# Kernel optimization log

Measured on AMD Instinct MI355X. Metric: run time of the kernel, lower is better.

## Reference

```python
import jax, jax.numpy as jnp
import numpy as np

DIM, HEADS, WIN, SHIFT = 384, 12, 7, 3
H, W = 56, 56
HEAD_DIM = DIM // HEADS
SCALE = HEAD_DIM ** -0.5
N = WIN * WIN


def _relative_index():
    coords = np.stack(np.meshgrid(np.arange(WIN), np.arange(WIN), indexing='ij')).reshape(2, -1)
    rel = (coords[:, :, None] - coords[:, None, :]).transpose(1, 2, 0)
    rel[:, :, 0] += WIN - 1
    rel[:, :, 1] += WIN - 1
    rel[:, :, 0] *= 2 * WIN - 1
    return rel.sum(-1)  # [N, N] int


def _attn_mask():
    img = np.zeros((H, W), dtype=np.float32)
    cnt = 0
    sls = (slice(0, -WIN), slice(-WIN, -SHIFT), slice(-SHIFT, None))
    for hs in sls:
        for ws in sls:
            img[hs, ws] = cnt
            cnt += 1
    m = img.reshape(H // WIN, WIN, W // WIN, WIN).transpose(0, 2, 1, 3).reshape(-1, N)  # [nw, N]
    diff = m[:, None, :] - m[:, :, None]  # [nw, N, N]
    return np.where(diff != 0, -10000.0, 0.0).astype(np.float32)

REL_IDX = jnp.asarray(_relative_index())
MASK = jnp.asarray(_attn_mask())  # [nw, N, N]


def _layernorm(x, w, b):
    mu = x.mean(-1, keepdims=True)
    var = ((x - mu) ** 2).mean(-1, keepdims=True)
    return (x - mu) * jax.lax.rsqrt(var + 1e-5) * w + b


def _window_partition(x):  # [B,H,W,C] -> [B*nw, N, C]
    B, _, _, C = x.shape
    x = x.reshape(B, H // WIN, WIN, W // WIN, WIN, C)
    x = x.transpose(0, 1, 3, 2, 4, 5)
    return x.reshape(-1, N, C)


def _window_reverse(w, B):  # [B*nw, N, C] -> [B,H,W,C]
    C = w.shape[-1]
    x = w.reshape(B, H // WIN, W // WIN, WIN, WIN, C)
    x = x.transpose(0, 1, 3, 2, 4, 5)
    return x.reshape(B, H, W, C)


def setup_inputs() -> dict:
    key = jax.random.key(0)
    ks = jax.random.split(key, 12)
    s = DIM ** -0.5
    return {
        'x': jax.random.normal(ks[0], (32, H * W, DIM), jnp.float32),
        'qkv_w': jax.random.normal(ks[1], (DIM, 3 * DIM), jnp.float32) * s,  # stored [in,out]
        'qkv_b': jnp.zeros((3 * DIM,), jnp.float32),
        'proj_w': jax.random.normal(ks[2], (DIM, DIM), jnp.float32) * s,
        'proj_b': jnp.zeros((DIM,), jnp.float32),
        'rel_bias': jax.random.normal(ks[3], ((2 * WIN - 1) ** 2, HEADS), jnp.float32) * 0.02,
        'norm1_w': jnp.ones((DIM,), jnp.float32),
        'norm1_b': jnp.zeros((DIM,), jnp.float32),
        'norm2_w': jnp.ones((DIM,), jnp.float32),
        'norm2_b': jnp.zeros((DIM,), jnp.float32),
        'mlp_w1': jax.random.normal(ks[4], (DIM, 4 * DIM), jnp.float32) * s,
        'mlp_b1': jnp.zeros((4 * DIM,), jnp.float32),
        'mlp_w2': jax.random.normal(ks[5], (4 * DIM, DIM), jnp.float32) * (4 * DIM) ** -0.5,
        'mlp_b2': jnp.zeros((DIM,), jnp.float32),
    }


def _forward(x, qkv_w, qkv_b, proj_w, proj_b, rel_bias, norm1_w, norm1_b,
             norm2_w, norm2_b, mlp_w1, mlp_b1, mlp_w2, mlp_b2):
    B, L, C = x.shape
    residual = x
    h = _layernorm(x, norm1_w, norm1_b).reshape(B, H, W, C)
    h = jnp.roll(h, (-SHIFT, -SHIFT), axis=(1, 2))
    wx = _window_partition(h)  # [B_, N, C]
    B_ = wx.shape[0]

    qkv = (wx @ qkv_w + qkv_b).reshape(B_, N, 3, HEADS, HEAD_DIM)
    q, k, v = qkv[:, :, 0], qkv[:, :, 1], qkv[:, :, 2]  # [B_, N, h, d]
    attn = jnp.einsum('bnhd,bmhd->bhnm', q * SCALE, k)  # [B_, h, N, N]
    rb = rel_bias[REL_IDX.reshape(-1)].reshape(N, N, HEADS).transpose(2, 0, 1)
    attn = attn + rb[None]
    nw = MASK.shape[0]
    attn = attn.reshape(B_ // nw, nw, HEADS, N, N) + MASK[None, :, None]
    attn = jax.nn.softmax(attn.reshape(B_, HEADS, N, N), axis=-1)
    out = jnp.einsum('bhnm,bmhd->bnhd', attn, v).reshape(B_, N, C)
    out = out @ proj_w + proj_b

    h = _window_reverse(out, B)
    h = jnp.roll(h, (SHIFT, SHIFT), axis=(1, 2))
    x = h.reshape(B, L, C) + residual

    m = _layernorm(x, norm2_w, norm2_b)
    m = jax.nn.gelu(m @ mlp_w1 + mlp_b1, approximate=False) @ mlp_w2 + mlp_b2
    return x + m


def reference(x, qkv_w, qkv_b, proj_w, proj_b, rel_bias, norm1_w, norm1_b,
              norm2_w, norm2_b, mlp_w1, mlp_b1, mlp_w2, mlp_b2):
    return _forward(x, qkv_w, qkv_b, proj_w, proj_b, rel_bias, norm1_w, norm1_b,
                    norm2_w, norm2_b, mlp_w1, mlp_b1, mlp_w2, mlp_b2)
```

## Files before the change

### kernel.cpp

```cpp
#include <hip/hip_runtime.h>
#include <hip/hip_bf16.h>

typedef unsigned short u16;
typedef __bf16 bf16x8 __attribute__((ext_vector_type(8)));
typedef float f32x4 __attribute__((ext_vector_type(4)));

#define HH 56
#define WW 56
#define DIM 384
#define NTOK 100352
#define NWIN 2048
#define NN 49

__device__ __forceinline__ u16 f2bf(float f) {
    __hip_bfloat16 h = __float2bfloat16(f);
    return *reinterpret_cast<u16*>(&h);
}
__device__ __forceinline__ float bf2f(u16 u) {
    union { unsigned int i; float f; } c; c.i = ((unsigned int)u) << 16; return c.f;
}

__device__ __forceinline__ float fast_gelu(float x) {
    float au = fabsf(x) * 0.70710678118654752f;
    float t = __builtin_amdgcn_rcpf(fmaf(0.3275911f, au, 1.0f));
    float p = fmaf(t, 1.061405429f, -1.453152027f);
    p = fmaf(t, p, 1.421413741f);
    p = fmaf(t, p, -0.284496736f);
    p = fmaf(t, p, 0.254829592f);
    p = p * t;
    float e = __expf(-au * au);
    float erfau = fmaf(-p, e, 1.0f);
    float erfx = __builtin_copysignf(erfau, x);
    return 0.5f * x * (1.0f + erfx);
}

#define GLD_LDS(gp, lp) __builtin_amdgcn_global_load_lds( \
    (const __attribute__((address_space(1))) void*)(gp), \
    (__attribute__((address_space(3))) void*)(lp), 16, 0, 0)

__global__ void castT(const float* __restrict__ in, u16* __restrict__ out, int K, int N) {
    int i = blockIdx.x * 256 + threadIdx.x;
    if (i < N * K) {
        int n = i / K, kk = i - n * K;
        out[i] = f2bf(in[(size_t)kk * N + n]);
    }
}

__global__ void bias_kernel(const float* __restrict__ rel_bias, float* __restrict__ Tb) {
    int ty = blockIdx.x / 12, h = blockIdx.x - ty * 12;
    for (int i = threadIdx.x; i < 4096; i += 256) {
        int q = i >> 6, kk = i & 63;
        float v;
        if (kk >= 49) v = -1e30f;
        else if (q >= 49) v = 0.f;
        else {
            int rn = q / 7, cn = q - rn * 7;
            int rm = kk / 7, cm = kk - rm * 7;
            float rb = rel_bias[((rn - rm + 6) * 13 + (cn - cm + 6)) * 12 + h];
            int h0 = (ty >> 1) ? 49 : 0;
            int w0 = (ty & 1) ? 49 : 0;
            int hn = h0 + rn, hm = h0 + rm, wn = w0 + cn, wm = w0 + cm;
            int regn = (hn < 49 ? 0 : (hn < 53 ? 1 : 2)) * 3 + (wn < 49 ? 0 : (wn < 53 ? 1 : 2));
            int regm = (hm < 49 ? 0 : (hm < 53 ? 1 : 2)) * 3 + (wm < 49 ? 0 : (wm < 53 ? 1 : 2));
            v = rb + ((regn == regm) ? 0.f : -10000.f);
        }
        Tb[(size_t)blockIdx.x * 4096 + i] = v;
    }
}

template<bool WIN_MAP>
__global__ __launch_bounds__(256) void ln_kernel(
    const float* __restrict__ x, const float* __restrict__ w, const float* __restrict__ b,
    u16* __restrict__ out)
{
    int token = blockIdx.x * 4 + (threadIdx.x >> 6);
    int lane = threadIdx.x & 63;
    const float* row = x + (size_t)token * DIM;
    float v[6]; float sum = 0.f, sq = 0.f;
#pragma unroll
    for (int j = 0; j < 3; j++) {
        float2 p = *(const float2*)(row + lane * 2 + j * 128);
        v[2*j] = p.x; v[2*j+1] = p.y;
        sum += p.x + p.y; sq += p.x * p.x + p.y * p.y;
    }
#pragma unroll
    for (int off = 32; off; off >>= 1) { sum += __shfl_xor(sum, off); sq += __shfl_xor(sq, off); }
    float mu = sum * (1.f / DIM);
    float rstd = rsqrtf(sq * (1.f / DIM) - mu * mu + 1e-5f);
    size_t obase;
    if (WIN_MAP) {
        int b_ = token / 3136, hw = token - b_ * 3136;
        int h = hw / WW, wc_ = hw - h * WW;
        int hr = h - 3; if (hr < 0) hr += HH;
        int wr = wc_ - 3; if (wr < 0) wr += WW;
        int win = b_ * 64 + (hr / 7) * 8 + (wr / 7);
        int n = (hr % 7) * 7 + (wr % 7);
        obase = ((size_t)win * NN + n) * DIM;
    } else {
        obase = (size_t)token * DIM;
    }
#pragma unroll
    for (int j = 0; j < 3; j++) {
        int c = lane * 2 + j * 128;
        float a0 = (v[2*j]   - mu) * rstd * w[c]   + b[c];
        float a1 = (v[2*j+1] - mu) * rstd * w[c+1] + b[c+1];
        unsigned int pair = (unsigned int)f2bf(a0) | ((unsigned int)f2bf(a1) << 16);
        *(unsigned int*)(out + obase + c) = pair;
    }
}

template<int EPI, int NT>
__global__ __launch_bounds__(256, 3) void gemm_kernel(
    const u16* __restrict__ A, const u16* __restrict__ Bt,
    const float* __restrict__ bias, const float* __restrict__ resid,
    void* __restrict__ outp, int N, int BNT)
{
    const int K = NT * 32;
    __shared__ u16 sA[3][4096];
    __shared__ u16 sB[3][4096];
    const int tid = threadIdx.x;
    const int lane = tid & 63;
    const int wave = tid >> 6;
    const int wr = wave >> 1, wc = wave & 1;

    const int q8 = gridDim.x >> 3;
    const int wg = (blockIdx.x & 7) * q8 + (blockIdx.x >> 3);
    const int bm = wg / BNT, bn = wg - bm * BNT;

    f32x4 acc[4][4] = {};

    const int r0 = tid >> 2;
    const int sg = (tid & 3) ^ (r0 & 3) ^ ((r0 >> 2) & 3);
    const u16* Arow0 = A + (size_t)(bm * 128 + r0) * K + sg * 8;
    const u16* Arow1 = Arow0 + (size_t)64 * K;
    const u16* Brow0 = Bt + (size_t)(bn * 128 + r0) * K + sg * 8;
    const u16* Brow1 = Brow0 + (size_t)64 * K;

#define STAGE(t, buf) do { \
        GLD_LDS(Arow0 + (t) * 32, &sA[buf][wave * 512]); \
        GLD_LDS(Arow1 + (t) * 32, &sA[buf][2048 + wave * 512]); \
        GLD_LDS(Brow0 + (t) * 32, &sB[buf][wave * 512]); \
        GLD_LDS(Brow1 + (t) * 32, &sB[buf][2048 + wave * 512]); \
    } while (0)

    STAGE(0, 0); STAGE(1, 1);

    const int l15 = lane & 15, g = lane >> 4;
    const int ssr = (g ^ (l15 & 3) ^ ((l15 >> 2) & 3)) * 8;

#pragma unroll
    for (int t = 0; t < NT; t++) {
        const int buf = t % 3;
        if (t + 1 < NT) asm volatile("s_waitcnt vmcnt(4)" ::: "memory");
        else            asm volatile("s_waitcnt vmcnt(0)" ::: "memory");
        __builtin_amdgcn_s_barrier();
        __builtin_amdgcn_sched_barrier(0);
        if (t + 2 < NT) STAGE(t + 2, (t + 2) % 3);
        bf16x8 af[4], bfr[4];
#pragma unroll
        for (int m = 0; m < 4; m++) {
            int row = wr * 64 + m * 16 + l15;
            af[m] = *(const bf16x8*)&sA[buf][row * 32 + ssr];
        }
#pragma unroll
        for (int n = 0; n < 4; n++) {
            int row = wc * 64 + n * 16 + l15;
            bfr[n] = *(const bf16x8*)&sB[buf][row * 32 + ssr];
        }
#pragma unroll
        for (int m = 0; m < 4; m++)
#pragma unroll
            for (int n = 0; n < 4; n++)
                acc[m][n] = __builtin_amdgcn_mfma_f32_16x16x32_bf16(bfr[n], af[m], acc[m][n], 0, 0, 0);
    }
#undef STAGE

    const int cb0 = bn * 128 + wc * 64 + g * 4;
    float4 bias4[4];
#pragma unroll
    for (int n = 0; n < 4; n++) bias4[n] = *(const float4*)(bias + cb0 + n * 16);

#pragma unroll
    for (int m = 0; m < 4; m++) {
        int row = bm * 128 + wr * 64 + m * 16 + l15;
        size_t obase;
        if (EPI == 1) {
            int win = row / NN, n = row - win * NN;
            int b_ = win >> 6, wi = win & 63;
            int hr = (wi >> 3) * 7 + n / 7;
            int wcl = (wi & 7) * 7 + n % 7;
            int hf = hr + 3; if (hf >= HH) hf -= HH;
            int wf = wcl + 3; if (wf >= WW) wf -= WW;
            obase = ((size_t)b_ * 3136 + hf * WW + wf) * DIM;
        } else {
            obase = (size_t)row * N;
        }
#pragma unroll
        for (int n = 0; n < 4; n++) {
            int col = cb0 + n * 16;
            float v0 = acc[m][n][0] + bias4[n].x;
            float v1 = acc[m][n][1] + bias4[n].y;
            float v2 = acc[m][n][2] + bias4[n].z;
            float v3 = acc[m][n][3] + bias4[n].w;
            if (EPI == 0 || EPI == 2) {
                if (EPI == 2) { v0 = fast_gelu(v0); v1 = fast_gelu(v1); v2 = fast_gelu(v2); v3 = fast_gelu(v3); }
                uint2 pk;
                pk.x = (unsigned int)f2bf(v0) | ((unsigned int)f2bf(v1) << 16);
                pk.y = (unsigned int)f2bf(v2) | ((unsigned int)f2bf(v3) << 16);
                *(uint2*)((u16*)outp + obase + col) = pk;
            } else {
                const float4 rs = *(const float4*)(resid + obase + col);
                float4 o;
                o.x = v0 + rs.x; o.y = v1 + rs.y; o.z = v2 + rs.z; o.w = v3 + rs.w;
                *(float4*)((float*)outp + obase + col) = o;
            }
        }
    }
}

__global__ __launch_bounds__(256) void attn_kernel(
    const u16* __restrict__ qkv, const float* __restrict__ Tb,
    u16* __restrict__ attn_out)
{
    __shared__ u16 smem[4][6912];
    const int win = blockIdx.x;
    const int wave = threadIdx.x >> 6;
    const int lane = threadIdx.x & 63;
    const int head = blockIdx.y * 4 + wave;
    const int l15 = lane & 15, g = lane >> 4;

    u16* Vt = smem[wave];
    u16* P  = Vt + 2304;

    const u16* qkvw = qkv + (size_t)win * NN * 1152 + head * 32;

    {
        int m = lane;
        bool real = m < NN;
        const u16* vrow = qkvw + (size_t)(real ? m : 0) * 1152 + 768;
        int4 z = {0,0,0,0};
        int4 c0 = real ? *(const int4*)(vrow)      : z;
        int4 c1 = real ? *(const int4*)(vrow + 8)  : z;
        int4 c2 = real ? *(const int4*)(vrow + 16) : z;
        int4 c3 = real ? *(const int4*)(vrow + 24) : z;
        u16 vals[32];
        *(int4*)&vals[0]  = c0; *(int4*)&vals[8]  = c1;
        *(int4*)&vals[16] = c2; *(int4*)&vals[24] = c3;
#pragma unroll
        for (int d = 0; d < 32; d++) Vt[d * 72 + m] = vals[d];
    }

    bf16x8 kf[4], qf[4];
#pragma unroll
    for (int t = 0; t < 4; t++) {
        int row = t * 16 + l15; if (row > 48) row = 48;
        const u16* base = qkvw + (size_t)row * 1152 + g * 8;
        kf[t] = *(const bf16x8*)(base + 384);
        qf[t] = *(const bf16x8*)(base);
    }
    f32x4 s[4][4];
#pragma unroll
    for (int mt = 0; mt < 4; mt++)
#pragma unroll
        for (int nt = 0; nt < 4; nt++) {
            f32x4 zero = {};
            s[mt][nt] = __builtin_amdgcn_mfma_f32_16x16x32_bf16(kf[mt], qf[nt], zero, 0, 0, 0);
        }

    const int wi = win & 63;
    const int ty = (((wi >> 3) == 7) ? 2 : 0) + (((wi & 7) == 7) ? 1 : 0);
    const float* tbb = Tb + (((size_t)ty * 12 + head) << 12);
    const float SCALE = 0.17677669529663687f;
#pragma unroll
    for (int nt = 0; nt < 4; nt++) {
        int q = nt * 16 + l15;
        const float* trow = tbb + q * 64 + g * 4;
        f32x4 b[4];
#pragma unroll
        for (int mt = 0; mt < 4; mt++) b[mt] = *(const f32x4*)(trow + mt * 16);
        float mx = -3e38f;
#pragma unroll
        for (int mt = 0; mt < 4; mt++)
#pragma unroll
            for (int r = 0; r < 4; r++) {
                float v = s[mt][nt][r] * SCALE + b[mt][r];
                s[mt][nt][r] = v;
                mx = fmaxf(mx, v);
            }
        mx = fmaxf(mx, __shfl_xor(mx, 16));
        mx = fmaxf(mx, __shfl_xor(mx, 32));
        float sum = 0.f;
#pragma unroll
        for (int mt = 0; mt < 4; mt++)
#pragma unroll
            for (int r = 0; r < 4; r++) {
                float e = __expf(s[mt][nt][r] - mx);
                s[mt][nt][r] = e;
                sum += e;
            }
        sum += __shfl_xor(sum, 16);
        sum += __shfl_xor(sum, 32);
        float inv = 1.f / sum;
#pragma unroll
        for (int mt = 0; mt < 4; mt++) {
            unsigned int p01 = (unsigned int)f2bf(s[mt][nt][0] * inv) | ((unsigned int)f2bf(s[mt][nt][1] * inv) << 16);
            unsigned int p23 = (unsigned int)f2bf(s[mt][nt][2] * inv) | ((unsigned int)f2bf(s[mt][nt][3] * inv) << 16);
            uint2 pk; pk.x = p01; pk.y = p23;
            *(uint2*)&P[(unsigned)q * 72 + mt * 16 + g * 4] = pk;
        }
    }

    bf16x8 vf[2][2];
#pragma unroll
    for (int ks = 0; ks < 2; ks++)
#pragma unroll
        for (int dt = 0; dt < 2; dt++)
            vf[ks][dt] = *(const bf16x8*)&Vt[(dt * 16 + l15) * 72 + ks * 32 + g * 8];

    f32x4 o[4][2] = {};
#pragma unroll
    for (int nt = 0; nt < 4; nt++) {
        bf16x8 pf0 = *(const bf16x8*)&P[(nt * 16 + l15) * 72 + g * 8];
        bf16x8 pf1 = *(const bf16x8*)&P[(nt * 16 + l15) * 72 + 32 + g * 8];
#pragma unroll
        for (int dt = 0; dt < 2; dt++) {
            o[nt][dt] = __builtin_amdgcn_mfma_f32_16x16x32_bf16(pf0, vf[0][dt], o[nt][dt], 0, 0, 0);
            o[nt][dt] = __builtin_amdgcn_mfma_f32_16x16x32_bf16(pf1, vf[1][dt], o[nt][dt], 0, 0, 0);
        }
    }

#pragma unroll
    for (int nt = 0; nt < 4; nt++)
#pragma unroll
        for (int r = 0; r < 4; r++) {
            int q = nt * 16 + 4 * g + r;
            if (q < NN) {
                size_t ob = ((size_t)win * NN + q) * DIM + head * 32;
                attn_out[ob + l15]      = f2bf(o[nt][0][r]);
                attn_out[ob + 16 + l15] = f2bf(o[nt][1][r]);
            }
        }
}

extern "C" void kernel_launch(void* const* d_in, const int* in_sizes, int n_in,
                              void* d_out, int out_size, void* d_ws, size_t ws_size,
                              hipStream_t stream)
{
    const float* x      = (const float*)d_in[0];
    const float* qkv_w  = (const float*)d_in[1];
    const float* qkv_b  = (const float*)d_in[2];
    const float* proj_w = (const float*)d_in[3];
    const float* proj_b = (const float*)d_in[4];
    const float* rel_b  = (const float*)d_in[5];
    const float* n1w    = (const float*)d_in[6];
    const float* n1b    = (const float*)d_in[7];
    const float* n2w    = (const float*)d_in[8];
    const float* n2b    = (const float*)d_in[9];
    const float* w1     = (const float*)d_in[10];
    const float* b1     = (const float*)d_in[11];
    const float* w2     = (const float*)d_in[12];
    const float* b2     = (const float*)d_in[13];

    char* ws = (char*)d_ws;
    u16* hidden  = (u16*)(ws);
    u16* qkvbuf  = hidden;
    float* Tb    = (float*)(ws + 231211008);
    u16* wxbuf   = (u16*)(ws + 308281344);
    u16* qkv_wt  = (u16*)(ws + 385351680);
    u16* proj_wt = (u16*)(ws + 386236416);
    u16* w1t     = (u16*)(ws + 386531328);
    u16* w2t     = (u16*)(ws + 387710976);

    castT<<<(1152*384 + 255) / 256, 256, 0, stream>>>(qkv_w, qkv_wt, 384, 1152);
    castT<<<(384*384  + 255) / 256, 256, 0, stream>>>(proj_w, proj_wt, 384, 384);
    castT<<<(384*1536 + 255) / 256, 256, 0, stream>>>(w1, w1t, 384, 1536);
    castT<<<(1536*384 + 255) / 256, 256, 0, stream>>>(w2, w2t, 1536, 384);
    bias_kernel<<<48, 256, 0, stream>>>(rel_b, Tb);

    ln_kernel<true><<<NTOK / 4, 256, 0, stream>>>(x, n1w, n1b, wxbuf);
    gemm_kernel<0, 12><<<784 * 9, 256, 0, stream>>>(wxbuf, qkv_wt, qkv_b, nullptr, qkvbuf, 1152, 9);
    attn_kernel<<<dim3(NWIN, 3), 256, 0, stream>>>(qkvbuf, Tb, wxbuf);
    gemm_kernel<1, 12><<<784 * 3, 256, 0, stream>>>(wxbuf, proj_wt, proj_b, x, d_out, 384, 3);
    ln_kernel<false><<<NTOK / 4, 256, 0, stream>>>((const float*)d_out, n2w, n2b, wxbuf);
    gemm_kernel<2, 12><<<784 * 12, 256, 0, stream>>>(wxbuf, w1t, b1, nullptr, hidden, 1536, 12);
    gemm_kernel<3, 48><<<784 * 3, 256, 0, stream>>>(hidden, w2t, b2, (const float*)d_out, d_out, 384, 3);
}
```

Before: 962.9 us.

## Load GEMM B operand directly from global into registers, bypassing LDS

The B (weight) tile is no longer staged through shared memory. Each wave now loads its own B fragments straight into registers with global_load_dwordx4, double-buffered across k-steps, while A keeps the triple-buffered LDS pipeline. This halves LDS footprint and LDS reads, and launch bounds are raised to 4 blocks per CU to use the freed space for occupancy. In exchange, B data is fetched redundantly by both wave rows, uses uncoalesced row-strided global loads, and needs more VGPRs and hand-tuned vmcnt waits.

```diff
diff --git a/kernel.cpp b/kernel.cpp
--- a/kernel.cpp
+++ b/kernel.cpp
@@ -110,14 +110,13 @@
 }
 
 template<int EPI, int NT>
-__global__ __launch_bounds__(256, 3) void gemm_kernel(
+__global__ __launch_bounds__(256, 4) void gemm_kernel(
     const u16* __restrict__ A, const u16* __restrict__ Bt,
     const float* __restrict__ bias, const float* __restrict__ resid,
     void* __restrict__ outp, int N, int BNT)
 {
     const int K = NT * 32;
     __shared__ u16 sA[3][4096];
-    __shared__ u16 sB[3][4096];
     const int tid = threadIdx.x;
     const int lane = tid & 63;
     const int wave = tid >> 6;
@@ -133,47 +132,59 @@
     const int sg = (tid & 3) ^ (r0 & 3) ^ ((r0 >> 2) & 3);
     const u16* Arow0 = A + (size_t)(bm * 128 + r0) * K + sg * 8;
     const u16* Arow1 = Arow0 + (size_t)64 * K;
-    const u16* Brow0 = Bt + (size_t)(bn * 128 + r0) * K + sg * 8;
-    const u16* Brow1 = Brow0 + (size_t)64 * K;
-
-#define STAGE(t, buf) do { \
+
+    const int l15 = lane & 15, g = lane >> 4;
+    const u16* Brow[4];
+#pragma unroll
+    for (int n = 0; n < 4; n++)
+        Brow[n] = Bt + (size_t)(bn * 128 + wc * 64 + n * 16 + l15) * K + g * 8;
+
+#define STAGE_A(t, buf) do { \
         GLD_LDS(Arow0 + (t) * 32, &sA[buf][wave * 512]); \
         GLD_LDS(Arow1 + (t) * 32, &sA[buf][2048 + wave * 512]); \
-        GLD_LDS(Brow0 + (t) * 32, &sB[buf][wave * 512]); \
-        GLD_LDS(Brow1 + (t) * 32, &sB[buf][2048 + wave * 512]); \
     } while (0)
 
-    STAGE(0, 0); STAGE(1, 1);
-
-    const int l15 = lane & 15, g = lane >> 4;
+#define LOADB(t, arr) do { \
+        asm volatile("global_load_dwordx4 %0, %1, off" : "=&v"(arr[0]) : "v"(Brow[0] + (t) * 32) : "memory"); \
+        asm volatile("global_load_dwordx4 %0, %1, off" : "=&v"(arr[1]) : "v"(Brow[1] + (t) * 32) : "memory"); \
+        asm volatile("global_load_dwordx4 %0, %1, off" : "=&v"(arr[2]) : "v"(Brow[2] + (t) * 32) : "memory"); \
+        asm volatile("global_load_dwordx4 %0, %1, off" : "=&v"(arr[3]) : "v"(Brow[3] + (t) * 32) : "memory"); \
+    } while (0)
+
+    int4 b0[4], b1[4];
+    STAGE_A(0, 0);
+    STAGE_A(1, 1);
+    LOADB(0, b0);
+
     const int ssr = (g ^ (l15 & 3) ^ ((l15 >> 2) & 3)) * 8;
 
 #pragma unroll
     for (int t = 0; t < NT; t++) {
         const int buf = t % 3;
-        if (t + 1 < NT) asm volatile("s_waitcnt vmcnt(4)" ::: "memory");
-        else            asm volatile("s_waitcnt vmcnt(0)" ::: "memory");
+        if (t + 1 < NT) asm volatile("s_waitcnt vmcnt(6)" ::: "memory");
+        else            asm volatile("s_waitcnt vmcnt(4)" ::: "memory");
         __builtin_amdgcn_s_barrier();
         __builtin_amdgcn_sched_barrier(0);
-        if (t + 2 < NT) STAGE(t + 2, (t + 2) % 3);
-        bf16x8 af[4], bfr[4];
+        if (t + 2 < NT) STAGE_A(t + 2, (t + 2) % 3);
+        if (t + 1 < NT) { if ((t & 1) == 0) LOADB(t + 1, b1); else LOADB(t + 1, b0); }
+        if (t + 2 < NT)      asm volatile("s_waitcnt vmcnt(6)" ::: "memory");
+        else if (t + 1 < NT) asm volatile("s_waitcnt vmcnt(4)" ::: "memory");
+        else                 asm volatile("s_waitcnt vmcnt(0)" ::: "memory");
+        __builtin_amdgcn_sched_barrier(0);
+        const int4* bc = ((t & 1) == 0) ? b0 : b1;
 #pragma unroll
         for (int m = 0; m < 4; m++) {
             int row = wr * 64 + m * 16 + l15;
-            af[m] = *(const bf16x8*)&sA[buf][row * 32 + ssr];
-        }
-#pragma unroll
-        for (int n = 0; n < 4; n++) {
-            int row = wc * 64 + n * 16 + l15;
-            bfr[n] = *(const bf16x8*)&sB[buf][row * 32 + ssr];
-        }
-#pragma unroll
-        for (int m = 0; m < 4; m++)
-#pragma unroll
-            for (int n = 0; n < 4; n++)
-                acc[m][n] = __builtin_amdgcn_mfma_f32_16x16x32_bf16(bfr[n], af[m], acc[m][n], 0, 0, 0);
-    }
-#undef STAGE
+            bf16x8 af = *(const bf16x8*)&sA[buf][row * 32 + ssr];
+#pragma unroll
+            for (int n = 0; n < 4; n++) {
+                bf16x8 bfr = *(const bf16x8*)&bc[n];
+                acc[m][n] = __builtin_amdgcn_mfma_f32_16x16x32_bf16(bfr, af, acc[m][n], 0, 0, 0);
+            }
+        }
+    }
+#undef STAGE_A
+#undef LOADB
 
     const int cb0 = bn * 128 + wc * 64 + g * 4;
     float4 bias4[4];
```

After: 1.239 ms. +28.7%, slower.
